# Kernel tuning notes

Hardware: AMD Instinct MI355X
Metric: run time of the kernel (lower is better)

The kernel has to match this reference:

```python
import jax, jax.numpy as jnp
import numpy as np

B, T, D, H = 2, 2048, 1024, 16
DH = D // H


def setup_inputs() -> dict:
    key = jax.random.key(0)
    ks = jax.random.split(key, 5)
    s = 1.0 / np.sqrt(D)
    return {
        "x": jax.random.normal(ks[0], (B, T, D), dtype=jnp.float32),
        "Wq": jax.random.normal(ks[1], (D, D), dtype=jnp.float32) * s,
        "Wk": jax.random.normal(ks[2], (D, D), dtype=jnp.float32) * s,
        "Wv": jax.random.normal(ks[3], (D, D), dtype=jnp.float32) * s,
        "Wo": jax.random.normal(ks[4], (D, D), dtype=jnp.float32) * s,
    }


def reference(x, Wq, Wk, Wv, Wo):
    # torch nn.Linear(bias=False): y = x @ W.T, weight shape [out, in]
    q = (x @ Wq.T).reshape(B, T, H, DH).transpose(0, 2, 1, 3)  # [B,H,T,Dh]
    k = (x @ Wk.T).reshape(B, T, H, DH).transpose(0, 2, 1, 3)
    v = (x @ Wv.T).reshape(B, T, H, DH).transpose(0, 2, 1, 3)
    scores = jnp.einsum("bhqd,bhkd->bhqk", q, k) / jnp.sqrt(jnp.float32(DH))
    att = jax.nn.softmax(scores, axis=-1)
    y = jnp.einsum("bhqk,bhkd->bhqd", att, v)  # [B,H,T,Dh]
    y = y.transpose(0, 2, 1, 3).reshape(B, T, D)
    return y @ Wo.T
```

## Files before the change

### kernel.cpp

```cpp
#include <hip/hip_runtime.h>
#include <math.h>

typedef __attribute__((ext_vector_type(8))) _Float16 half8;
typedef __attribute__((ext_vector_type(4))) _Float16 half4;
typedef __attribute__((ext_vector_type(4))) float f32x4;

namespace {
constexpr int T_ = 2048, DH_ = 64;
constexpr int M_ = 4096;
constexpr int KD = 1024;
}

__global__ __launch_bounds__(256)
void conv_half4(const float* __restrict__ s0, const float* __restrict__ s1,
                const float* __restrict__ s2, const float* __restrict__ s3,
                _Float16* __restrict__ dst)
{
    const float* s = (blockIdx.y == 0) ? s0 : (blockIdx.y == 1) ? s1
                   : (blockIdx.y == 2) ? s2 : s3;
    const size_t i = ((size_t)blockIdx.x * 256 + threadIdx.x) * 8;
    const float4 a = *reinterpret_cast<const float4*>(s + i);
    const float4 b = *reinterpret_cast<const float4*>(s + i + 4);
    half8 h;
    h[0] = (_Float16)a.x; h[1] = (_Float16)a.y; h[2] = (_Float16)a.z; h[3] = (_Float16)a.w;
    h[4] = (_Float16)b.x; h[5] = (_Float16)b.y; h[6] = (_Float16)b.z; h[7] = (_Float16)b.w;
    *reinterpret_cast<half8*>(dst + (size_t)blockIdx.y * 1048576 + i) = h;
}

template <int BN>
__global__ __launch_bounds__(256)
void gemm_half(const _Float16* __restrict__ A, const _Float16* __restrict__ Bw,
               float* __restrict__ Cout,
               _Float16* __restrict__ qh, _Float16* __restrict__ kh,
               _Float16* __restrict__ vh, const int mode)
{
    constexpr int NF = BN / 32;
    __shared__ _Float16 As[128 * 64];
    __shared__ _Float16 Bs[BN * 64];
    const int tid = threadIdx.x;
    const int l   = tid & 63;
    const int w   = tid >> 6;
    const int wm  = w >> 1, wn = w & 1;
    const int m0  = blockIdx.y * 128;
    const int n0  = blockIdx.x * BN;

    f32x4 acc[4][NF];
#pragma unroll
    for (int i = 0; i < 4; ++i)
#pragma unroll
        for (int j = 0; j < NF; ++j) acc[i][j] = (f32x4){0.f, 0.f, 0.f, 0.f};

    const int srow = l >> 3;
    const int scol = ((l & 7) ^ srow) << 3;
    const int frow = l & 15;
    const int fkb  = (l >> 4) << 4;

    for (int kt = 0; kt < 16; ++kt) {
        const int kOff = kt << 6;
#pragma unroll
        for (int s = 0; s < 4; ++s) {
            const int j = (w << 2) + s;
            const _Float16* gp = A + (size_t)(m0 + (j << 3) + srow) * KD + kOff + scol;
            __builtin_amdgcn_global_load_lds(
                (const __attribute__((address_space(1))) void*)gp,
                (__attribute__((address_space(3))) void*)(As + (j << 9)), 16, 0, 0);
        }
#pragma unroll
        for (int s = 0; s < BN / 32; ++s) {
            const int j = w * (BN / 32) + s;
            const _Float16* gp = Bw + (size_t)(n0 + (j << 3) + srow) * KD + kOff + scol;
            __builtin_amdgcn_global_load_lds(
                (const __attribute__((address_space(1))) void*)gp,
                (__attribute__((address_space(3))) void*)(Bs + (j << 9)), 16, 0, 0);
        }
        __syncthreads();
#pragma unroll
        for (int ks = 0; ks < 2; ++ks) {
            half8 af[4], bfr[NF];
#pragma unroll
            for (int fi = 0; fi < 4; ++fi) {
                const int row = wm * 64 + fi * 16 + frow;
                const int cb  = (ks * 64 + fkb) ^ ((row & 7) << 4);
                af[fi] = *reinterpret_cast<const half8*>(
                    reinterpret_cast<const char*>(As) + row * 128 + cb);
            }
#pragma unroll
            for (int fj = 0; fj < NF; ++fj) {
                const int row = wn * (NF * 16) + fj * 16 + frow;
                const int cb  = (ks * 64 + fkb) ^ ((row & 7) << 4);
                bfr[fj] = *reinterpret_cast<const half8*>(
                    reinterpret_cast<const char*>(Bs) + row * 128 + cb);
            }
#pragma unroll
            for (int fi = 0; fi < 4; ++fi)
#pragma unroll
                for (int fj = 0; fj < NF; ++fj)
                    acc[fi][fj] = __builtin_amdgcn_mfma_f32_16x16x32_f16(
                        af[fi], bfr[fj], acc[fi][fj], 0, 0, 0);
        }
        __syncthreads();
    }

    const int r0 = (l >> 4) << 2;
    const float QSC = 0.125f * 1.44269504f;
#pragma unroll
    for (int fi = 0; fi < 4; ++fi)
#pragma unroll
        for (int fj = 0; fj < NF; ++fj) {
            const int mb = m0 + wm * 64 + fi * 16 + r0;
            const int n  = n0 + wn * (NF * 16) + fj * 16 + (l & 15);
            if (mode == 0) {
                const int bb = mb >> 11, tb = mb & 2047;
                const int which = n >> 10, nl = n & 1023;
                const int hh = nl >> 6, dh = nl & 63;
                const int bh = (bb << 4) + hh;
                if (which == 0) {
#pragma unroll
                    for (int r = 0; r < 4; ++r)
                        qh[(((size_t)bh << 11) + tb + r) * 64 + dh] =
                            (_Float16)(acc[fi][fj][r] * QSC);
                } else if (which == 1) {
#pragma unroll
                    for (int r = 0; r < 4; ++r)
                        kh[(((size_t)bh << 11) + tb + r) * 64 + dh] =
                            (_Float16)acc[fi][fj][r];
                } else {
                    half4 v4;
#pragma unroll
                    for (int r = 0; r < 4; ++r) v4[r] = (_Float16)acc[fi][fj][r];
                    *reinterpret_cast<half4*>(
                        &vh[(((size_t)bh << 6) + dh) * 2048 + tb]) = v4;
                }
            } else {
#pragma unroll
                for (int r = 0; r < 4; ++r)
                    Cout[(size_t)(mb + r) * 1024 + n] = acc[fi][fj][r];
            }
        }
}

#define SWZ(row, bytecol) (((row) << 7) + ((bytecol) ^ (((row) & 7) << 4)))

__global__ __launch_bounds__(256)
void attn_mfma(const _Float16* __restrict__ Qh, const _Float16* __restrict__ Kh,
               const _Float16* __restrict__ Vh, _Float16* __restrict__ Yh)
{
    __shared__ _Float16 Ks[2][64 * 64];
    __shared__ _Float16 Vs[2][64 * 64];
    __shared__ _Float16 Ps[128 * 64];
    const int tid = threadIdx.x;
    const int l   = tid & 63;
    const int w   = tid >> 6;
    const int g4  = l >> 4;
    const int c16 = l & 15;
    const int bh  = blockIdx.y;
    const int t0  = blockIdx.x * 128;
    const size_t qkbase = (size_t)bh * T_ * DH_;
    const size_t vbase  = (size_t)bh * DH_ * T_;

    const int srow = l >> 3;
    const int scol = ((l & 7) ^ srow) << 3;

    half8 qf[2][2];
#pragma unroll
    for (int c = 0; c < 2; ++c)
#pragma unroll
        for (int ks = 0; ks < 2; ++ks)
            qf[c][ks] = *reinterpret_cast<const half8*>(
                Qh + qkbase + (size_t)(t0 + 32 * w + 16 * c + c16) * 64
                    + ks * 32 + g4 * 8);

    half8 ones;
#pragma unroll
    for (int j = 0; j < 8; ++j) ones[j] = (_Float16)1.f;

#pragma unroll
    for (int s = 0; s < 2; ++s) {
        const int j   = (w << 1) + s;
        const int row = (j << 3) + srow;
        const _Float16* gk = Kh + qkbase + (size_t)row * 64 + scol;
        __builtin_amdgcn_global_load_lds(
            (const __attribute__((address_space(1))) void*)gk,
            (__attribute__((address_space(3))) void*)(&Ks[0][0] + (j << 9)), 16, 0, 0);
        const _Float16* gv = Vh + vbase + (size_t)row * T_ + scol;
        __builtin_amdgcn_global_load_lds(
            (const __attribute__((address_space(1))) void*)gv,
            (__attribute__((address_space(3))) void*)(&Vs[0][0] + (j << 9)), 16, 0, 0);
    }
    __syncthreads();

    f32x4 o[2][4], ol[2];
#pragma unroll
    for (int c = 0; c < 2; ++c) {
#pragma unroll
        for (int i = 0; i < 4; ++i) o[c][i] = (f32x4){0.f, 0.f, 0.f, 0.f};
        ol[c] = (f32x4){0.f, 0.f, 0.f, 0.f};
    }

    for (int ktile = 0; ktile < T_ / 64; ++ktile) {
        const int cur = ktile & 1;
        if (ktile + 1 < T_ / 64) {
            const int nxt = cur ^ 1;
#pragma unroll
            for (int s = 0; s < 2; ++s) {
                const int j   = (w << 1) + s;
                const int row = (j << 3) + srow;
                const _Float16* gk = Kh + qkbase +
                    (size_t)((ktile + 1) * 64 + row) * 64 + scol;
                __builtin_amdgcn_global_load_lds(
                    (const __attribute__((address_space(1))) void*)gk,
                    (__attribute__((address_space(3))) void*)(&Ks[nxt][0] + (j << 9)), 16, 0, 0);
                const _Float16* gv = Vh + vbase + (size_t)row * T_ +
                    (ktile + 1) * 64 + scol;
                __builtin_amdgcn_global_load_lds(
                    (const __attribute__((address_space(1))) void*)gv,
                    (__attribute__((address_space(3))) void*)(&Vs[nxt][0] + (j << 9)), 16, 0, 0);
            }
        }

        const char* ksBase = reinterpret_cast<const char*>(&Ks[cur][0]);
        const char* vsBase = reinterpret_cast<const char*>(&Vs[cur][0]);
        f32x4 s[2][4];
#pragma unroll
        for (int c = 0; c < 2; ++c)
#pragma unroll
            for (int fj = 0; fj < 4; ++fj) s[c][fj] = (f32x4){0.f, 0.f, 0.f, 0.f};
        __builtin_amdgcn_s_setprio(1);
#pragma unroll
        for (int ks = 0; ks < 2; ++ks)
#pragma unroll
            for (int fj = 0; fj < 4; ++fj) {
                const int row = fj * 16 + c16;
                const half8 kf = *reinterpret_cast<const half8*>(
                    ksBase + SWZ(row, ks * 64 + (g4 << 4)));
                s[0][fj] = __builtin_amdgcn_mfma_f32_16x16x32_f16(kf, qf[0][ks], s[0][fj], 0, 0, 0);
                s[1][fj] = __builtin_amdgcn_mfma_f32_16x16x32_f16(kf, qf[1][ks], s[1][fj], 0, 0, 0);
            }
        __builtin_amdgcn_s_setprio(0);

#pragma unroll
        for (int c = 0; c < 2; ++c) {
            const int q = 32 * w + 16 * c + c16;
#pragma unroll
            for (int fj = 0; fj < 4; ++fj) {
                half4 p4;
#pragma unroll
                for (int r4 = 0; r4 < 4; ++r4)
                    p4[r4] = (_Float16)__builtin_amdgcn_exp2f(s[c][fj][r4]);
                *reinterpret_cast<half4*>(reinterpret_cast<char*>(Ps) +
                    SWZ(q, fj * 32 + (g4 << 3))) = p4;
            }
        }

        __builtin_amdgcn_s_setprio(1);
#pragma unroll
        for (int ks = 0; ks < 2; ++ks) {
            const half8 pf0 = *reinterpret_cast<const half8*>(
                reinterpret_cast<const char*>(Ps) + SWZ(32 * w + c16, ks * 64 + (g4 << 4)));
            const half8 pf1 = *reinterpret_cast<const half8*>(
                reinterpret_cast<const char*>(Ps) + SWZ(32 * w + 16 + c16, ks * 64 + (g4 << 4)));
#pragma unroll
            for (int fj = 0; fj < 4; ++fj) {
                const int vrow = fj * 16 + c16;
                const half8 vf = *reinterpret_cast<const half8*>(
                    vsBase + SWZ(vrow, ks * 64 + (g4 << 4)));
                o[0][fj] = __builtin_amdgcn_mfma_f32_16x16x32_f16(pf0, vf, o[0][fj], 0, 0, 0);
                o[1][fj] = __builtin_amdgcn_mfma_f32_16x16x32_f16(pf1, vf, o[1][fj], 0, 0, 0);
            }
            ol[0] = __builtin_amdgcn_mfma_f32_16x16x32_f16(pf0, ones, ol[0], 0, 0, 0);
            ol[1] = __builtin_amdgcn_mfma_f32_16x16x32_f16(pf1, ones, ol[1], 0, 0, 0);
        }
        __builtin_amdgcn_s_setprio(0);

        __syncthreads();
    }

    const int bb = bh >> 4, hh = bh & 15;
#pragma unroll
    for (int c = 0; c < 2; ++c)
#pragma unroll
        for (int r4 = 0; r4 < 4; ++r4) {
            const int t = t0 + 32 * w + 16 * c + (g4 << 2) + r4;
            const float inv = 1.f / ol[c][r4];
            const size_t mrow = ((size_t)bb * T_ + t) * 1024;
#pragma unroll
            for (int fj = 0; fj < 4; ++fj) {
                const int col = hh * 64 + fj * 16 + c16;
                Yh[mrow + col] = (_Float16)(o[c][fj][r4] * inv);
            }
        }
}

extern "C" void kernel_launch(void* const* d_in, const int* in_sizes, int n_in,
                              void* d_out, int out_size, void* d_ws, size_t ws_size,
                              hipStream_t stream)
{
    const float* x  = (const float*)d_in[0];
    const float* Wq = (const float*)d_in[1];
    const float* Wk = (const float*)d_in[2];
    const float* Wv = (const float*)d_in[3];
    const float* Wo = (const float*)d_in[4];

    unsigned char* ws = (unsigned char*)d_ws;
    _Float16* xh = (_Float16*)ws;
    _Float16* wh = (_Float16*)(ws + (size_t) 8388608);
    _Float16* qh = (_Float16*)(ws + (size_t)16777216);
    _Float16* kh = (_Float16*)(ws + (size_t)25165824);
    _Float16* vh = (_Float16*)(ws + (size_t)33554432);
    _Float16* yh = xh;

    conv_half4<<<dim3(2048, 1), 256, 0, stream>>>(x, nullptr, nullptr, nullptr, xh);
    conv_half4<<<dim3(512, 4), 256, 0, stream>>>(Wq, Wk, Wv, Wo, wh);

    dim3 blk(256);
    dim3 g1(24, 32);
    gemm_half<128><<<g1, blk, 0, stream>>>(xh, wh, nullptr, qh, kh, vh, 0);

    dim3 ga(T_ / 128, 32);
    attn_mfma<<<ga, blk, 0, stream>>>(qh, kh, vh, yh);

    dim3 g2(16, 32);
    gemm_half<64><<<g2, blk, 0, stream>>>(yh, wh + (size_t)3072 * KD, (float*)d_out,
                                          nullptr, nullptr, nullptr, 1);
}
```

Measured before the change: 127.3 us.

## Split attention key range across two blocks and add partial-sum reduce kernel

The attention kernel grid gains a z dimension of 2, so each block processes half of the key tiles and writes unnormalized fp16 partial outputs and fp32 row sums to workspace. A new reduce kernel adds the two partials, divides by the combined row sum and writes the normalized head output into the [B,T,D] layout. The goal is twice as many blocks in flight on the GPU, which should hide memory latency better and balance load. The cost is a fp16 round-trip of partial outputs through global memory plus an extra kernel launch. Summing partials is only correct if the exponentials share a fixed scale rather than a per-block running max.

```diff
diff --git a/kernel.cpp b/kernel.cpp
--- a/kernel.cpp
+++ b/kernel.cpp
@@ -143,7 +143,8 @@
 
 __global__ __launch_bounds__(256)
 void attn_mfma(const _Float16* __restrict__ Qh, const _Float16* __restrict__ Kh,
-               const _Float16* __restrict__ Vh, _Float16* __restrict__ Yh)
+               const _Float16* __restrict__ Vh,
+               _Float16* __restrict__ Opart, float* __restrict__ Lpart)
 {
     __shared__ _Float16 Ks[2][64 * 64];
     __shared__ _Float16 Vs[2][64 * 64];
@@ -154,7 +155,9 @@
     const int g4  = l >> 4;
     const int c16 = l & 15;
     const int bh  = blockIdx.y;
+    const int z   = blockIdx.z;
     const int t0  = blockIdx.x * 128;
+    const int kt0 = z << 4;
     const size_t qkbase = (size_t)bh * T_ * DH_;
     const size_t vbase  = (size_t)bh * DH_ * T_;
 
@@ -178,11 +181,11 @@
     for (int s = 0; s < 2; ++s) {
         const int j   = (w << 1) + s;
         const int row = (j << 3) + srow;
-        const _Float16* gk = Kh + qkbase + (size_t)row * 64 + scol;
+        const _Float16* gk = Kh + qkbase + (size_t)(kt0 * 64 + row) * 64 + scol;
         __builtin_amdgcn_global_load_lds(
             (const __attribute__((address_space(1))) void*)gk,
             (__attribute__((address_space(3))) void*)(&Ks[0][0] + (j << 9)), 16, 0, 0);
-        const _Float16* gv = Vh + vbase + (size_t)row * T_ + scol;
+        const _Float16* gv = Vh + vbase + (size_t)row * T_ + kt0 * 64 + scol;
         __builtin_amdgcn_global_load_lds(
             (const __attribute__((address_space(1))) void*)gv,
             (__attribute__((address_space(3))) void*)(&Vs[0][0] + (j << 9)), 16, 0, 0);
@@ -197,9 +200,9 @@
         ol[c] = (f32x4){0.f, 0.f, 0.f, 0.f};
     }
 
-    for (int ktile = 0; ktile < T_ / 64; ++ktile) {
+    for (int ktile = kt0; ktile < kt0 + 16; ++ktile) {
         const int cur = ktile & 1;
-        if (ktile + 1 < T_ / 64) {
+        if (ktile + 1 < kt0 + 16) {
             const int nxt = cur ^ 1;
 #pragma unroll
             for (int s = 0; s < 2; ++s) {
@@ -275,20 +278,45 @@
         __syncthreads();
     }
 
-    const int bb = bh >> 4, hh = bh & 15;
+    const size_t pbase = ((size_t)(z * 32 + bh)) * 2048;
 #pragma unroll
     for (int c = 0; c < 2; ++c)
 #pragma unroll
         for (int r4 = 0; r4 < 4; ++r4) {
             const int t = t0 + 32 * w + 16 * c + (g4 << 2) + r4;
-            const float inv = 1.f / ol[c][r4];
-            const size_t mrow = ((size_t)bb * T_ + t) * 1024;
-#pragma unroll
-            for (int fj = 0; fj < 4; ++fj) {
-                const int col = hh * 64 + fj * 16 + c16;
-                Yh[mrow + col] = (_Float16)(o[c][fj][r4] * inv);
-            }
-        }
+            const size_t orow = (pbase + t) * 64;
+#pragma unroll
+            for (int fj = 0; fj < 4; ++fj)
+                Opart[orow + fj * 16 + c16] = (_Float16)o[c][fj][r4];
+            if (c16 == 0) Lpart[pbase + t] = ol[c][r4];
+        }
+}
+
+__global__ __launch_bounds__(256)
+void attn_reduce(const _Float16* __restrict__ Opart,
+                 const float* __restrict__ Lpart, _Float16* __restrict__ Yh)
+{
+    const int idx = blockIdx.x * 256 + threadIdx.x;
+    const int bh  = idx >> 11;
+    const int t   = idx & 2047;
+    const int bb  = bh >> 4, hh = bh & 15;
+    const half8* r0 = reinterpret_cast<const half8*>(
+        Opart + ((size_t)bh * 2048 + t) * 64);
+    const half8* r1 = reinterpret_cast<const half8*>(
+        Opart + ((size_t)(32 + bh) * 2048 + t) * 64);
+    const float inv = 1.f / (Lpart[(size_t)bh * 2048 + t]
+                           + Lpart[(size_t)(32 + bh) * 2048 + t]);
+    half8* dst = reinterpret_cast<half8*>(
+        Yh + ((size_t)bb * 2048 + t) * 1024 + hh * 64);
+#pragma unroll
+    for (int j = 0; j < 8; ++j) {
+        const half8 a = r0[j], b = r1[j];
+        half8 y;
+#pragma unroll
+        for (int e = 0; e < 8; ++e)
+            y[e] = (_Float16)(((float)a[e] + (float)b[e]) * inv);
+        dst[j] = y;
+    }
 }
 
 extern "C" void kernel_launch(void* const* d_in, const int* in_sizes, int n_in,
@@ -307,6 +335,8 @@
     _Float16* qh = (_Float16*)(ws + (size_t)16777216);
     _Float16* kh = (_Float16*)(ws + (size_t)25165824);
     _Float16* vh = (_Float16*)(ws + (size_t)33554432);
+    _Float16* op = (_Float16*)(ws + (size_t)41943040);
+    float*    lp = (float*)   (ws + (size_t)58720256);
     _Float16* yh = xh;
 
     conv_half4<<<dim3(2048, 1), 256, 0, stream>>>(x, nullptr, nullptr, nullptr, xh);
@@ -316,8 +346,10 @@
     dim3 g1(24, 32);
     gemm_half<128><<<g1, blk, 0, stream>>>(xh, wh, nullptr, qh, kh, vh, 0);
 
-    dim3 ga(T_ / 128, 32);
-    attn_mfma<<<ga, blk, 0, stream>>>(qh, kh, vh, yh);
+    dim3 ga(T_ / 128, 32, 2);
+    attn_mfma<<<ga, blk, 0, stream>>>(qh, kh, vh, op, lp);
+
+    attn_reduce<<<256, 256, 0, stream>>>(op, lp, yh);
 
     dim3 g2(16, 32);
     gemm_half<64><<<g2, blk, 0, stream>>>(yh, wh + (size_t)3072 * KD, (float*)d_out,
```

Result: slower. 137.9 us (+8.3%).
